# Performance work log

Measured on AMD Instinct MI355X. Metric: run time of the kernel, lower is better.

The kernel has to match this reference:

```python
import jax, jax.numpy as jnp
import numpy as np

WINDOW_SIZE = 11
SIGMA = 1.5
C1 = 0.01 ** 2
C2 = 0.03 ** 2


def _gaussian_window(window_size, channel):
    coords = jnp.arange(window_size, dtype=jnp.float32) - window_size // 2
    g = jnp.exp(-(coords ** 2) / (2.0 * SIGMA ** 2))
    g = g / g.sum()
    w2d = jnp.outer(g, g)  # [K, K]
    # depthwise conv kernel, OIHW with I=1 (feature_group_count=channel)
    return jnp.broadcast_to(w2d[None, None], (channel, 1, window_size, window_size))


def _depthwise_conv(x, window):
    pad = WINDOW_SIZE // 2
    return jax.lax.conv_general_dilated(
        x, window,
        window_strides=(1, 1),
        padding=((pad, pad), (pad, pad)),
        dimension_numbers=('NCHW', 'OIHW', 'NCHW'),
        feature_group_count=x.shape[1],
    )


def setup_inputs() -> dict:
    key = jax.random.key(0)
    k1, k2 = jax.random.split(key)
    shape = (32, 1, 512, 512)
    img1 = jax.random.uniform(k1, shape, dtype=jnp.float32)
    img2 = jax.random.uniform(k2, shape, dtype=jnp.float32)
    return {"img1": img1, "img2": img2}


def reference(img1, img2):
    channel = img1.shape[1]
    window = _gaussian_window(WINDOW_SIZE, channel).astype(img1.dtype)
    mu1 = _depthwise_conv(img1, window)
    mu2 = _depthwise_conv(img2, window)
    mu1_sq = mu1 * mu1
    mu2_sq = mu2 * mu2
    mu1_mu2 = mu1 * mu2
    sigma1_sq = _depthwise_conv(img1 * img1, window) - mu1_sq
    sigma2_sq = _depthwise_conv(img2 * img2, window) - mu2_sq
    sigma12 = _depthwise_conv(img1 * img2, window) - mu1_mu2
    ssim_map = ((2.0 * mu1_mu2 + C1) * (2.0 * sigma12 + C2)) / (
        (mu1_sq + mu2_sq + C1) * (sigma1_sq + sigma2_sq + C2))
    return 1.0 - ssim_map.mean()
```

## Files before the change

### kernel.cpp

```cpp
#include <hip/hip_runtime.h>

#define IMG   512
#define NIMG  32
#define TX    128
#define TY    16
#define NQ    36
#define VQS   17
#define VPL   (NQ * VQS)
#define VITEMS (NQ * 8)
#define NBX   (IMG / TX)
#define NBY   (IMG / TY)
#define NBLK  (NBX * NBY * NIMG)
#define NPIX  (32.0f * 512.0f * 512.0f)

constexpr float GW[11] = {
    0.00102838f, 0.00759876f, 0.03600077f, 0.10936069f, 0.21300553f,
    0.26601174f,
    0.21300553f, 0.10936069f, 0.03600077f, 0.00759876f, 0.00102838f
};
constexpr float C1c = 0.0001f;
constexpr float C2c = 0.0009f;

__global__ void ssim_init_out(float* __restrict__ out) { out[0] = 1.0f; }

__device__ __forceinline__ float4 f4mul(float4 a, float4 b) {
    return make_float4(a.x * b.x, a.y * b.y, a.z * b.z, a.w * b.w);
}
__device__ __forceinline__ float4 f4fma(float w, float4 v, float4 c) {
    return make_float4(fmaf(w, v.x, c.x), fmaf(w, v.y, c.y),
                       fmaf(w, v.z, c.z), fmaf(w, v.w, c.w));
}

template <bool INTERIOR>
__device__ __forceinline__ void vpass_item(int it, int X0, int Y0,
        const float* __restrict__ a0, const float* __restrict__ b0,
        float4* __restrict__ sV4) {
    const int q  = it % NQ;
    const int g  = it / NQ;
    const int y0 = 2 * g;
    int gx0 = X0 - 8 + 4 * q;
    const int gyb = Y0 + y0 - 5;
    bool okx = true;
    if (!INTERIOR) {
        okx = (gx0 >= 0) && (gx0 + 3 < IMG);
        gx0 = min(max(gx0, 0), IMG - 4);
    }

    float4 acc[5][2];
#pragma unroll
    for (int ch = 0; ch < 5; ++ch)
#pragma unroll
        for (int o = 0; o < 2; ++o)
            acc[ch][o] = make_float4(0.f, 0.f, 0.f, 0.f);

    float4 ra[6], rb[6];
#pragma unroll
    for (int half = 0; half < 2; ++half) {
#pragma unroll
        for (int j = 0; j < 6; ++j) {
            int gy = gyb + half * 6 + j;
            if (!INTERIOR) gy = min(max(gy, 0), IMG - 1);
            const int off = gy * IMG + gx0;
            ra[j] = *(const float4*)(a0 + off);
            rb[j] = *(const float4*)(b0 + off);
        }
#pragma unroll
        for (int j = 0; j < 6; ++j) {
            const int k = half * 6 + j;
            const float4 a = ra[j];
            const float4 b = rb[j];
            const float4 aa = f4mul(a, a);
            const float4 bb = f4mul(b, b);
            const float4 ab = f4mul(a, b);
            if (INTERIOR) {
                if (k <= 10) {
                    const float w = GW[k];
                    acc[0][0] = f4fma(w, a,  acc[0][0]);
                    acc[1][0] = f4fma(w, b,  acc[1][0]);
                    acc[2][0] = f4fma(w, aa, acc[2][0]);
                    acc[3][0] = f4fma(w, bb, acc[3][0]);
                    acc[4][0] = f4fma(w, ab, acc[4][0]);
                }
                if (k >= 1) {
                    const float w = GW[k - 1];
                    acc[0][1] = f4fma(w, a,  acc[0][1]);
                    acc[1][1] = f4fma(w, b,  acc[1][1]);
                    acc[2][1] = f4fma(w, aa, acc[2][1]);
                    acc[3][1] = f4fma(w, bb, acc[3][1]);
                    acc[4][1] = f4fma(w, ab, acc[4][1]);
                }
            } else {
                const int gy = gyb + k;
                const bool ok = okx && ((unsigned)gy < IMG);
                float w0 = (k <= 10) ? GW[k] : 0.0f;
                float w1 = (k >= 1) ? GW[k - 1] : 0.0f;
                w0 = ok ? w0 : 0.0f;
                w1 = ok ? w1 : 0.0f;
                acc[0][0] = f4fma(w0, a,  acc[0][0]);
                acc[1][0] = f4fma(w0, b,  acc[1][0]);
                acc[2][0] = f4fma(w0, aa, acc[2][0]);
                acc[3][0] = f4fma(w0, bb, acc[3][0]);
                acc[4][0] = f4fma(w0, ab, acc[4][0]);
                acc[0][1] = f4fma(w1, a,  acc[0][1]);
                acc[1][1] = f4fma(w1, b,  acc[1][1]);
                acc[2][1] = f4fma(w1, aa, acc[2][1]);
                acc[3][1] = f4fma(w1, bb, acc[3][1]);
                acc[4][1] = f4fma(w1, ab, acc[4][1]);
            }
        }
    }
#pragma unroll
    for (int o = 0; o < 2; ++o)
#pragma unroll
        for (int ch = 0; ch < 5; ++ch)
            sV4[ch * VPL + q * VQS + (y0 + o)] = acc[ch][o];
}

__global__ __launch_bounds__(256, 3) void ssim_fused(
        const float* __restrict__ img1, const float* __restrict__ img2,
        float* __restrict__ ws, float* __restrict__ out) {
    __shared__ float4 sV4[5 * VPL];

    const int tid = threadIdx.x;
    const int X0 = blockIdx.x * TX;
    const int Y0 = blockIdx.y * TY;
    const int n  = blockIdx.z;
    const float* a0 = img1 + (size_t)n * IMG * IMG;
    const float* b0 = img2 + (size_t)n * IMG * IMG;

    const bool interior = (X0 >= 8) && (X0 - 8 + 4 * (NQ - 1) + 3 < IMG) &&
                          (Y0 >= 5) && (Y0 + TY + 4 < IMG);

    if (interior) {
        for (int it = tid; it < VITEMS; it += 256)
            vpass_item<true>(it, X0, Y0, a0, b0, sV4);
    } else {
        for (int it = tid; it < VITEMS; it += 256)
            vpass_item<false>(it, X0, Y0, a0, b0, sV4);
    }
    __syncthreads();

    float sum = 0.0f;
    {
        const int y   = tid & 15;
        const int grp = tid >> 4;
        float res[5][8];
#pragma unroll
        for (int ch = 0; ch < 5; ++ch) {
            const float4* base = &sV4[ch * VPL + y];
            float v[24];
#pragma unroll
            for (int d = 0; d < 6; ++d) {
                const float4 t = base[(2 * grp + d) * VQS];
                v[4 * d + 0] = t.x; v[4 * d + 1] = t.y;
                v[4 * d + 2] = t.z; v[4 * d + 3] = t.w;
            }
#pragma unroll
            for (int e = 0; e < 8; ++e) {
                float s = GW[0] * v[e + 3];
#pragma unroll
                for (int k = 1; k < 11; ++k) s = fmaf(GW[k], v[e + 3 + k], s);
                res[ch][e] = s;
            }
        }
#pragma unroll
        for (int e = 0; e < 8; ++e) {
            const float mu1 = res[0][e], mu2 = res[1][e];
            const float m1s = mu1 * mu1;
            const float m2s = mu2 * mu2;
            const float m12 = mu1 * mu2;
            const float s1  = res[2][e] - m1s;
            const float s2  = res[3][e] - m2s;
            const float s12 = res[4][e] - m12;
            const float num = (2.0f * m12 + C1c) * (2.0f * s12 + C2c);
            const float den = (m1s + m2s + C1c) * (s1 + s2 + C2c);
            sum += num * __builtin_amdgcn_rcpf(den);
        }
    }

#pragma unroll
    for (int off = 32; off > 0; off >>= 1)
        sum += __shfl_down(sum, off, 64);

    __shared__ float wred[4];
    if ((tid & 63) == 0) wred[tid >> 6] = sum;
    __syncthreads();
    if (tid == 0) {
        const float s = wred[0] + wred[1] + wred[2] + wred[3];
        if (ws) {
            const int bid = blockIdx.x +
                (int)gridDim.x * (blockIdx.y + (int)gridDim.y * blockIdx.z);
            ws[bid] = s;
        } else {
            atomicAdd(out, -s * (1.0f / NPIX));
        }
    }
}

__global__ __launch_bounds__(1024) void ssim_reduce(
        const float* __restrict__ ws, float* __restrict__ out) {
    const int t = threadIdx.x;
    float s = 0.0f;
    for (int i = t; i < NBLK; i += 1024) s += ws[i];
#pragma unroll
    for (int off = 32; off > 0; off >>= 1)
        s += __shfl_down(s, off, 64);
    __shared__ float wr[16];
    if ((t & 63) == 0) wr[t >> 6] = s;
    __syncthreads();
    if (t < 64) {
        float v = (t < 16) ? wr[t] : 0.0f;
#pragma unroll
        for (int off = 8; off > 0; off >>= 1)
            v += __shfl_down(v, off, 64);
        if (t == 0) out[0] = 1.0f - v * (1.0f / NPIX);
    }
}

extern "C" void kernel_launch(void* const* d_in, const int* in_sizes, int n_in,
                              void* d_out, int out_size, void* d_ws, size_t ws_size,
                              hipStream_t stream) {
    const float* img1 = (const float*)d_in[0];
    const float* img2 = (const float*)d_in[1];
    float* out = (float*)d_out;
    const bool two_stage = (d_ws != nullptr) && (ws_size >= NBLK * sizeof(float));
    float* ws = two_stage ? (float*)d_ws : nullptr;

    if (!two_stage) ssim_init_out<<<1, 1, 0, stream>>>(out);

    dim3 grid(NBX, NBY, NIMG);
    ssim_fused<<<grid, 256, 0, stream>>>(img1, img2, ws, out);

    if (two_stage) ssim_reduce<<<1, 1024, 0, stream>>>(ws, out);
}
```

Measured before the change: 120.4 us.

## Store vertical-pass sums as packed fp16 and run horizontal pass in half2

Vertical-pass results for the five channels are converted to packed fp16 pairs and stored in a row-major shared-memory layout instead of float4 columns. The horizontal 11-tap pass then reads them with wide uint4 loads, builds odd-offset pairs with alignbit, and uses packed half2 FMAs. The goal is to halve shared-memory footprint and traffic, and to halve horizontal-pass ALU work. The cost is reduced precision: fp16 rounding and accumulation feeding the sigma = E[x²] − mu² subtraction may hurt SSIM accuracy.

Result: slower. 140.9 us (+17.0%).

```diff
diff --git a/kernel.cpp b/kernel.cpp
--- a/kernel.cpp
+++ b/kernel.cpp
@@ -1,12 +1,13 @@
 #include <hip/hip_runtime.h>
+#include <hip/hip_fp16.h>
 
 #define IMG   512
 #define NIMG  32
 #define TX    128
 #define TY    16
 #define NQ    36
-#define VQS   17
-#define VPL   (NQ * VQS)
+#define RSDW  76
+#define PLDW  (TY * RSDW)
 #define VITEMS (NQ * 8)
 #define NBX   (IMG / TX)
 #define NBY   (IMG / TY)
@@ -31,10 +32,25 @@
                        fmaf(w, v.z, c.z), fmaf(w, v.w, c.w));
 }
 
+__device__ __forceinline__ unsigned int pkrtz(float x, float y) {
+#if __has_builtin(__builtin_amdgcn_cvt_pkrtz)
+    typedef __attribute__((ext_vector_type(2))) __fp16 h2v;
+    h2v r = __builtin_amdgcn_cvt_pkrtz(x, y);
+    union { h2v h; unsigned int u; } c; c.h = r; return c.u;
+#else
+    __half2 h = __halves2half2(__float2half_rn(x), __float2half_rn(y));
+    union { __half2 h; unsigned int u; } c; c.h = h; return c.u;
+#endif
+}
+__device__ __forceinline__ __half2 u2h(unsigned int u) {
+    union { unsigned int u; __half2 h; } c; c.u = u; return c.h;
+}
+#define HWC(k) __half2half2(__float2half_rn(GW[k]))
+
 template <bool INTERIOR>
 __device__ __forceinline__ void vpass_item(int it, int X0, int Y0,
         const float* __restrict__ a0, const float* __restrict__ b0,
-        float4* __restrict__ sV4) {
+        unsigned int* __restrict__ sH) {
     const int q  = it % NQ;
     const int g  = it / NQ;
     const int y0 = 2 * g;
@@ -110,16 +126,23 @@
         }
     }
 #pragma unroll
-    for (int o = 0; o < 2; ++o)
-#pragma unroll
-        for (int ch = 0; ch < 5; ++ch)
-            sV4[ch * VPL + q * VQS + (y0 + o)] = acc[ch][o];
+    for (int o = 0; o < 2; ++o) {
+        const int y = y0 + o;
+#pragma unroll
+        for (int ch = 0; ch < 5; ++ch) {
+            const float4 A = acc[ch][o];
+            uint2 p;
+            p.x = pkrtz(A.x, A.y);
+            p.y = pkrtz(A.z, A.w);
+            *(uint2*)&sH[ch * PLDW + y * RSDW + 2 * q] = p;
+        }
+    }
 }
 
 __global__ __launch_bounds__(256, 3) void ssim_fused(
         const float* __restrict__ img1, const float* __restrict__ img2,
         float* __restrict__ ws, float* __restrict__ out) {
-    __shared__ float4 sV4[5 * VPL];
+    __shared__ unsigned int sH[5 * PLDW];
 
     const int tid = threadIdx.x;
     const int X0 = blockIdx.x * TX;
@@ -133,34 +156,46 @@
 
     if (interior) {
         for (int it = tid; it < VITEMS; it += 256)
-            vpass_item<true>(it, X0, Y0, a0, b0, sV4);
+            vpass_item<true>(it, X0, Y0, a0, b0, sH);
     } else {
         for (int it = tid; it < VITEMS; it += 256)
-            vpass_item<false>(it, X0, Y0, a0, b0, sV4);
+            vpass_item<false>(it, X0, Y0, a0, b0, sH);
     }
     __syncthreads();
 
     float sum = 0.0f;
     {
-        const int y   = tid & 15;
-        const int grp = tid >> 4;
+        const int y = tid & 15;
+        const int g = tid >> 4;
         float res[5][8];
 #pragma unroll
         for (int ch = 0; ch < 5; ++ch) {
-            const float4* base = &sV4[ch * VPL + y];
-            float v[24];
-#pragma unroll
-            for (int d = 0; d < 6; ++d) {
-                const float4 t = base[(2 * grp + d) * VQS];
-                v[4 * d + 0] = t.x; v[4 * d + 1] = t.y;
-                v[4 * d + 2] = t.z; v[4 * d + 3] = t.w;
-            }
-#pragma unroll
-            for (int e = 0; e < 8; ++e) {
-                float s = GW[0] * v[e + 3];
-#pragma unroll
-                for (int k = 1; k < 11; ++k) s = fmaf(GW[k], v[e + 3 + k], s);
-                res[ch][e] = s;
+            const unsigned int* base = &sH[ch * PLDW + y * RSDW + 4 * g];
+            const uint4 r0 = *(const uint4*)(base);
+            const uint4 r1 = *(const uint4*)(base + 4);
+            const uint4 r2 = *(const uint4*)(base + 8);
+            unsigned int v[12] = { r0.x, r0.y, r0.z, r0.w,
+                                   r1.x, r1.y, r1.z, r1.w,
+                                   r2.x, r2.y, r2.z, r2.w };
+            unsigned int sh[10];
+#pragma unroll
+            for (int m = 1; m <= 9; ++m)
+                sh[m] = __builtin_amdgcn_alignbit(v[m + 1], v[m], 16);
+#pragma unroll
+            for (int j = 0; j < 4; ++j) {
+                __half2 acc = __hmul2(HWC(0), u2h(sh[j + 1]));
+                acc = __hfma2(HWC(1),  u2h(v[j + 2]),  acc);
+                acc = __hfma2(HWC(2),  u2h(sh[j + 2]), acc);
+                acc = __hfma2(HWC(3),  u2h(v[j + 3]),  acc);
+                acc = __hfma2(HWC(4),  u2h(sh[j + 3]), acc);
+                acc = __hfma2(HWC(5),  u2h(v[j + 4]),  acc);
+                acc = __hfma2(HWC(6),  u2h(sh[j + 4]), acc);
+                acc = __hfma2(HWC(7),  u2h(v[j + 5]),  acc);
+                acc = __hfma2(HWC(8),  u2h(sh[j + 5]), acc);
+                acc = __hfma2(HWC(9),  u2h(v[j + 6]),  acc);
+                acc = __hfma2(HWC(10), u2h(sh[j + 6]), acc);
+                res[ch][2 * j]     = __low2float(acc);
+                res[ch][2 * j + 1] = __high2float(acc);
             }
         }
 #pragma unroll
```
